# Kernel tuning notes

Hardware: AMD Instinct MI355X
Metric: run time of the kernel (lower is better)

Reference implementation:

```python
import jax, jax.numpy as jnp
import numpy as np

N_NODES = 2048
N_EDGES = 32768
D_IN = 128      # input_dimension
D_MEM_H = 128   # mem_hidden_dimension
D_MEM_A = 128   # mem_agg_hidden_dimension
D_AGG_H = 128   # agg_hidden_dimension
D_OUT = 128     # output_dimension
D_FEAT = 32     # feature_dimension


def setup_inputs() -> dict:
    key = jax.random.key(0)
    ks = jax.random.split(key, 10)
    state = jax.random.normal(ks[0], (N_EDGES, D_IN), dtype=jnp.float32)
    feature = jax.random.normal(ks[1], (N_EDGES, D_FEAT), dtype=jnp.float32)
    mask = (jax.random.uniform(ks[2], (N_NODES, N_EDGES)) < 0.005).astype(jnp.float32)
    mask_transpose = mask.T
    s = 0.05
    W1_m = jax.random.normal(ks[3], (D_MEM_H, D_IN), dtype=jnp.float32) * s
    b1_m = jax.random.normal(ks[4], (D_MEM_H,), dtype=jnp.float32) * s
    W2_m = jax.random.normal(ks[5], (D_MEM_A, D_MEM_H), dtype=jnp.float32) * s
    W1_a = jax.random.normal(ks[6], (D_AGG_H, D_MEM_A + D_FEAT), dtype=jnp.float32) * s
    b1_a = jax.random.normal(ks[7], (D_AGG_H,), dtype=jnp.float32) * s
    W2_a = jax.random.normal(ks[8], (D_OUT, D_AGG_H), dtype=jnp.float32) * s
    return {"state": state, "feature": feature, "mask": mask,
            "mask_transpose": mask_transpose,
            "W1_m": W1_m, "b1_m": b1_m, "W2_m": W2_m,
            "W1_a": W1_a, "b1_a": b1_a, "W2_a": W2_a}


def reference(state, feature, mask, mask_transpose, W1_m, b1_m, W2_m, W1_a, b1_a, W2_a):
    ls = jax.nn.log_sigmoid
    # memory MLP: [E, D_IN] -> [E, D_MEM_A]
    s = ls(ls(state @ W1_m.T + b1_m) @ W2_m.T)
    # bipartite aggregation: gather per-node sums, scatter back to edges
    agg = mask_transpose @ (mask @ s) - s  # include_self_message=False
    # concat features and aggregation MLP: [E, D_MEM_A + D_FEAT] -> [E, D_OUT]
    agg = jnp.concatenate((agg, feature), axis=1)
    out = ls(ls(agg @ W1_a.T + b1_a) @ W2_a.T)
    return out
```

## Files before the change

### kernel.cpp

```cpp
#include <hip/hip_runtime.h>
#include <cstdint>
#include <cstddef>

#define N_NODES 2048
#define N_EDGES 32768
#define ROW_CAP 384
#define COL_CAP 48

typedef unsigned short u16;
typedef __bf16 bf16x8 __attribute__((ext_vector_type(8)));
typedef float f32x4 __attribute__((ext_vector_type(4)));

union BF8 {
  bf16x8 v;
  u16 s[8];
  uint4 q;
};

__device__ __forceinline__ u16 f2bf(float f) {
  uint32_t u = __float_as_uint(f);
  uint32_t r = (u + 0x7fffu + ((u >> 16) & 1u)) >> 16;
  return (u16)r;
}
__device__ __forceinline__ float bf2f(u16 h) {
  return __uint_as_float(((uint32_t)h) << 16);
}
__device__ __forceinline__ float logsig(float x) {
  return fminf(x, 0.0f) - __logf(1.0f + __expf(-fabsf(x)));
}

__global__ __launch_bounds__(256) void conv_weights(
    const float* __restrict__ W1m, const float* __restrict__ W2m,
    const float* __restrict__ W1a, const float* __restrict__ W2a,
    u16* __restrict__ wb)
{
  const int i = blockIdx.x * 256 + threadIdx.x;
  if (i < 16384)      wb[i] = f2bf(W1m[i]);
  else if (i < 32768) wb[i] = f2bf(W2m[i - 16384]);
  else if (i < 53248) wb[i] = f2bf(W1a[i - 32768]);
  else if (i < 69632) wb[i] = f2bf(W2a[i - 53248]);
}

__global__ __launch_bounds__(256) void mlp_m_kernel(
    const float* __restrict__ state, const u16* __restrict__ W1b,
    const float* __restrict__ b1, const u16* __restrict__ W2b,
    u16* __restrict__ s_out)
{
  const int tid = threadIdx.x;
  const int wave = tid >> 6;
  const int lane = tid & 63;
  const int l16 = lane & 15;
  const int quad = lane >> 4;
  const int row0 = blockIdx.x * 128;

  __shared__ u16 h_lds[128][136];

  const f32x4 vzero = {0.f, 0.f, 0.f, 0.f};
  f32x4 acc[2][8];
  for (int rt = 0; rt < 2; ++rt)
    for (int ct = 0; ct < 8; ++ct) acc[rt][ct] = vzero;

  for (int kc = 0; kc < 4; ++kc) {
    const int k0 = kc * 32 + quad * 8;
    BF8 a[2];
    for (int rt = 0; rt < 2; ++rt) {
      const float* ap = state + (size_t)(row0 + wave * 32 + rt * 16 + l16) * 128 + k0;
      const float4 f0 = ((const float4*)ap)[0];
      const float4 f1 = ((const float4*)ap)[1];
      a[rt].s[0] = f2bf(f0.x); a[rt].s[1] = f2bf(f0.y);
      a[rt].s[2] = f2bf(f0.z); a[rt].s[3] = f2bf(f0.w);
      a[rt].s[4] = f2bf(f1.x); a[rt].s[5] = f2bf(f1.y);
      a[rt].s[6] = f2bf(f1.z); a[rt].s[7] = f2bf(f1.w);
    }
    for (int ct = 0; ct < 8; ++ct) {
      BF8 b;
      b.q = *(const uint4*)(W1b + (size_t)(ct * 16 + l16) * 128 + k0);
      for (int rt = 0; rt < 2; ++rt)
        acc[rt][ct] = __builtin_amdgcn_mfma_f32_16x16x32_bf16(a[rt].v, b.v, acc[rt][ct], 0, 0, 0);
    }
  }

  for (int ct = 0; ct < 8; ++ct) {
    const int col = ct * 16 + l16;
    const float bias = b1[col];
    for (int rt = 0; rt < 2; ++rt) {
      const int r = wave * 32 + rt * 16 + quad * 4;
      for (int i = 0; i < 4; ++i)
        h_lds[r + i][col] = f2bf(logsig(acc[rt][ct][i] + bias));
    }
  }
  __syncthreads();

  f32x4 acc2[2][8];
  for (int rt = 0; rt < 2; ++rt)
    for (int ct = 0; ct < 8; ++ct) acc2[rt][ct] = vzero;

  for (int kc = 0; kc < 4; ++kc) {
    const int k0 = kc * 32 + quad * 8;
    BF8 a[2];
    for (int rt = 0; rt < 2; ++rt)
      a[rt].q = *(const uint4*)&h_lds[wave * 32 + rt * 16 + l16][k0];
    for (int ct = 0; ct < 8; ++ct) {
      BF8 b;
      b.q = *(const uint4*)(W2b + (size_t)(ct * 16 + l16) * 128 + k0);
      for (int rt = 0; rt < 2; ++rt)
        acc2[rt][ct] = __builtin_amdgcn_mfma_f32_16x16x32_bf16(a[rt].v, b.v, acc2[rt][ct], 0, 0, 0);
    }
  }

  for (int ct = 0; ct < 8; ++ct) {
    const int col = ct * 16 + l16;
    for (int rt = 0; rt < 2; ++rt) {
      const int r = row0 + wave * 32 + rt * 16 + quad * 4;
      for (int i = 0; i < 4; ++i)
        s_out[(size_t)(r + i) * 128 + col] = f2bf(logsig(acc2[rt][ct][i]));
    }
  }
}

__global__ __launch_bounds__(256) void scan_mask(
    const float* __restrict__ mask, int* __restrict__ row_cnt,
    int* __restrict__ row_edges, int* __restrict__ col_cnt,
    int* __restrict__ col_nodes)
{
  const int n = blockIdx.x;
  __shared__ int cnt;
  __shared__ int list[ROW_CAP];
  if (threadIdx.x == 0) cnt = 0;
  __syncthreads();

  const uint4* row = (const uint4*)(mask + (size_t)n * N_EDGES);
  for (int i = threadIdx.x; i < N_EDGES / 4; i += 256) {
    const uint4 v = row[i];
    const int e = i * 4;
    if (v.x) { int p = atomicAdd(&cnt, 1); if (p < ROW_CAP) list[p] = e; }
    if (v.y) { int p = atomicAdd(&cnt, 1); if (p < ROW_CAP) list[p] = e + 1; }
    if (v.z) { int p = atomicAdd(&cnt, 1); if (p < ROW_CAP) list[p] = e + 2; }
    if (v.w) { int p = atomicAdd(&cnt, 1); if (p < ROW_CAP) list[p] = e + 3; }
  }
  __syncthreads();

  const int c = min(cnt, ROW_CAP);
  if (threadIdx.x == 0) row_cnt[n] = c;
  for (int i = threadIdx.x; i < c; i += 256) {
    const int e = list[i];
    row_edges[(size_t)n * ROW_CAP + i] = e;
    const int slot = atomicAdd(&col_cnt[e], 1);
    if (slot < COL_CAP) col_nodes[(size_t)e * COL_CAP + slot] = n;
  }
}

__global__ __launch_bounds__(128) void pass_a(
    const u16* __restrict__ s_bf, const int* __restrict__ row_cnt,
    const int* __restrict__ row_edges, float* __restrict__ y)
{
  const int n = blockIdx.x;
  const int d = threadIdx.x;
  __shared__ int elist[ROW_CAP];
  const int cnt = row_cnt[n];
  for (int i = threadIdx.x; i < cnt; i += 128)
    elist[i] = row_edges[(size_t)n * ROW_CAP + i];
  __syncthreads();
  float acc = 0.f;
#pragma unroll 4
  for (int i = 0; i < cnt; ++i)
    acc += bf2f(s_bf[(size_t)elist[i] * 128 + d]);
  y[n * 128 + d] = acc;
}

__global__ __launch_bounds__(256) void pass_b(
    const float* __restrict__ y, const u16* __restrict__ s_bf,
    const float* __restrict__ feature, const int* __restrict__ col_cnt,
    const int* __restrict__ col_nodes, u16* __restrict__ cat)
{
  const int e = blockIdx.x * 2 + (threadIdx.x >> 7);
  const int d = threadIdx.x & 127;
  const int cnt = min(col_cnt[e], COL_CAP);
  const int* cn = col_nodes + (size_t)e * COL_CAP;
  float acc = 0.f;
#pragma unroll 2
  for (int j = 0; j < cnt; ++j)
    acc += y[cn[j] * 128 + d];
  acc -= bf2f(s_bf[(size_t)e * 128 + d]);
  cat[(size_t)e * 160 + d] = f2bf(acc);
  if (d < 32)
    cat[(size_t)e * 160 + 128 + d] = f2bf(feature[e * 32 + d]);
}

__global__ __launch_bounds__(256) void mlp_a_kernel(
    const u16* __restrict__ cat, const u16* __restrict__ W1b,
    const float* __restrict__ b1, const u16* __restrict__ W2b,
    float* __restrict__ out)
{
  const int tid = threadIdx.x;
  const int wave = tid >> 6;
  const int lane = tid & 63;
  const int l16 = lane & 15;
  const int quad = lane >> 4;
  const int row0 = blockIdx.x * 128;

  __shared__ u16 h_lds[128][136];

  const f32x4 vzero = {0.f, 0.f, 0.f, 0.f};
  f32x4 acc[2][8];
  for (int rt = 0; rt < 2; ++rt)
    for (int ct = 0; ct < 8; ++ct) acc[rt][ct] = vzero;

  for (int kc = 0; kc < 5; ++kc) {
    const int k0 = kc * 32 + quad * 8;
    BF8 a[2];
    for (int rt = 0; rt < 2; ++rt)
      a[rt].q = *(const uint4*)(cat + (size_t)(row0 + wave * 32 + rt * 16 + l16) * 160 + k0);
    for (int ct = 0; ct < 8; ++ct) {
      BF8 b;
      b.q = *(const uint4*)(W1b + (size_t)(ct * 16 + l16) * 160 + k0);
      for (int rt = 0; rt < 2; ++rt)
        acc[rt][ct] = __builtin_amdgcn_mfma_f32_16x16x32_bf16(a[rt].v, b.v, acc[rt][ct], 0, 0, 0);
    }
  }

  for (int ct = 0; ct < 8; ++ct) {
    const int col = ct * 16 + l16;
    const float bias = b1[col];
    for (int rt = 0; rt < 2; ++rt) {
      const int r = wave * 32 + rt * 16 + quad * 4;
      for (int i = 0; i < 4; ++i)
        h_lds[r + i][col] = f2bf(logsig(acc[rt][ct][i] + bias));
    }
  }
  __syncthreads();

  f32x4 acc2[2][8];
  for (int rt = 0; rt < 2; ++rt)
    for (int ct = 0; ct < 8; ++ct) acc2[rt][ct] = vzero;

  for (int kc = 0; kc < 4; ++kc) {
    const int k0 = kc * 32 + quad * 8;
    BF8 a[2];
    for (int rt = 0; rt < 2; ++rt)
      a[rt].q = *(const uint4*)&h_lds[wave * 32 + rt * 16 + l16][k0];
    for (int ct = 0; ct < 8; ++ct) {
      BF8 b;
      b.q = *(const uint4*)(W2b + (size_t)(ct * 16 + l16) * 128 + k0);
      for (int rt = 0; rt < 2; ++rt)
        acc2[rt][ct] = __builtin_amdgcn_mfma_f32_16x16x32_bf16(a[rt].v, b.v, acc2[rt][ct], 0, 0, 0);
    }
  }

  for (int ct = 0; ct < 8; ++ct) {
    const int col = ct * 16 + l16;
    for (int rt = 0; rt < 2; ++rt) {
      const int r = row0 + wave * 32 + rt * 16 + quad * 4;
      for (int i = 0; i < 4; ++i)
        out[(size_t)(r + i) * 128 + col] = logsig(acc2[rt][ct][i]);
    }
  }
}

extern "C" void kernel_launch(void* const* d_in, const int* in_sizes, int n_in,
                              void* d_out, int out_size, void* d_ws, size_t ws_size,
                              hipStream_t stream)
{
  const float* state   = (const float*)d_in[0];
  const float* feature = (const float*)d_in[1];
  const float* mask    = (const float*)d_in[2];
  const float* W1m = (const float*)d_in[4];
  const float* b1m = (const float*)d_in[5];
  const float* W2m = (const float*)d_in[6];
  const float* W1a = (const float*)d_in[7];
  const float* b1a = (const float*)d_in[8];
  const float* W2a = (const float*)d_in[9];
  float* out = (float*)d_out;

  char* ws = (char*)d_ws;
  u16*  s_bf      = (u16*)(ws);
  u16*  cat       = (u16*)(ws + 8388608);
  float* y        = (float*)(ws + 18874368);
  int*  row_cnt   = (int*)(ws + 19922944);
  int*  row_edges = (int*)(ws + 19931136);
  int*  col_cnt   = (int*)(ws + 23076864);
  int*  col_nodes = (int*)(ws + 23207936);
  u16*  wb        = (u16*)(ws + 29499392);

  hipMemsetAsync(col_cnt, 0, N_EDGES * sizeof(int), stream);
  conv_weights<<<272, 256, 0, stream>>>(W1m, W2m, W1a, W2a, wb);
  mlp_m_kernel<<<N_EDGES / 128, 256, 0, stream>>>(state, wb, b1m, wb + 16384, s_bf);
  scan_mask<<<N_NODES, 256, 0, stream>>>(mask, row_cnt, row_edges, col_cnt, col_nodes);
  pass_a<<<N_NODES, 128, 0, stream>>>(s_bf, row_cnt, row_edges, y);
  pass_b<<<N_EDGES / 2, 256, 0, stream>>>(y, s_bf, feature, col_cnt, col_nodes, cat);
  mlp_a_kernel<<<N_EDGES / 128, 256, 0, stream>>>(cat, wb + 32768, b1a, wb + 53248, out);
}
```

Baseline: 623.4 us.

## Fuse mask scan with memory MLP and aggregation scatter with agg MLP

Merges the memory MLP and mask scanning into one heterogeneous launch so the two independent stages run concurrently. The per-edge gather of node sums is fused into the aggregation MLP and stays in LDS, so the concatenated tensor never goes to global memory. The memset is folded into the weight conversion kernel, the mask scan uses wave ballots with one atomic per wave and nontemporal loads, and pass_a splits each node's edge list across two thread halves. The cost is more LDS per block in agg_mlp, which may lower occupancy, and a less coalesced per-wave gather.

Measured after the change: 687.6 us. 10.3% more time.

```diff
diff --git a/kernel.cpp b/kernel.cpp
--- a/kernel.cpp
+++ b/kernel.cpp
@@ -10,6 +10,7 @@
 typedef unsigned short u16;
 typedef __bf16 bf16x8 __attribute__((ext_vector_type(8)));
 typedef float f32x4 __attribute__((ext_vector_type(4)));
+typedef uint32_t u32x4 __attribute__((ext_vector_type(4)));
 
 union BF8 {
   bf16x8 v;
@@ -32,49 +33,212 @@
 __global__ __launch_bounds__(256) void conv_weights(
     const float* __restrict__ W1m, const float* __restrict__ W2m,
     const float* __restrict__ W1a, const float* __restrict__ W2a,
-    u16* __restrict__ wb)
+    u16* __restrict__ wb, int* __restrict__ col_cnt)
 {
   const int i = blockIdx.x * 256 + threadIdx.x;
+  if (i < N_EDGES) col_cnt[i] = 0;
   if (i < 16384)      wb[i] = f2bf(W1m[i]);
   else if (i < 32768) wb[i] = f2bf(W2m[i - 16384]);
   else if (i < 53248) wb[i] = f2bf(W1a[i - 32768]);
   else if (i < 69632) wb[i] = f2bf(W2a[i - 53248]);
 }
 
-__global__ __launch_bounds__(256) void mlp_m_kernel(
+__global__ __launch_bounds__(256) void mlp_scan(
     const float* __restrict__ state, const u16* __restrict__ W1b,
     const float* __restrict__ b1, const u16* __restrict__ W2b,
-    u16* __restrict__ s_out)
+    u16* __restrict__ s_out,
+    const float* __restrict__ mask, int* __restrict__ row_cnt,
+    int* __restrict__ row_edges, int* __restrict__ col_cnt,
+    int* __restrict__ col_nodes)
+{
+  const int tid = threadIdx.x;
+
+  __shared__ u16 h_lds[128][136];
+  __shared__ int cnt;
+  __shared__ int list[ROW_CAP];
+
+  if (blockIdx.x < 256) {
+    const int wave = tid >> 6;
+    const int lane = tid & 63;
+    const int l16 = lane & 15;
+    const int quad = lane >> 4;
+    const int row0 = blockIdx.x * 128;
+
+    const f32x4 vzero = {0.f, 0.f, 0.f, 0.f};
+    f32x4 acc[2][8];
+    for (int rt = 0; rt < 2; ++rt)
+      for (int ct = 0; ct < 8; ++ct) acc[rt][ct] = vzero;
+
+    for (int kc = 0; kc < 4; ++kc) {
+      const int k0 = kc * 32 + quad * 8;
+      BF8 a[2];
+      for (int rt = 0; rt < 2; ++rt) {
+        const float* ap = state + (size_t)(row0 + wave * 32 + rt * 16 + l16) * 128 + k0;
+        const float4 f0 = ((const float4*)ap)[0];
+        const float4 f1 = ((const float4*)ap)[1];
+        a[rt].s[0] = f2bf(f0.x); a[rt].s[1] = f2bf(f0.y);
+        a[rt].s[2] = f2bf(f0.z); a[rt].s[3] = f2bf(f0.w);
+        a[rt].s[4] = f2bf(f1.x); a[rt].s[5] = f2bf(f1.y);
+        a[rt].s[6] = f2bf(f1.z); a[rt].s[7] = f2bf(f1.w);
+      }
+      for (int ct = 0; ct < 8; ++ct) {
+        BF8 b;
+        b.q = *(const uint4*)(W1b + (size_t)(ct * 16 + l16) * 128 + k0);
+        for (int rt = 0; rt < 2; ++rt)
+          acc[rt][ct] = __builtin_amdgcn_mfma_f32_16x16x32_bf16(a[rt].v, b.v, acc[rt][ct], 0, 0, 0);
+      }
+    }
+
+    for (int ct = 0; ct < 8; ++ct) {
+      const int col = ct * 16 + l16;
+      const float bias = b1[col];
+      for (int rt = 0; rt < 2; ++rt) {
+        const int r = wave * 32 + rt * 16 + quad * 4;
+        for (int i = 0; i < 4; ++i)
+          h_lds[r + i][col] = f2bf(logsig(acc[rt][ct][i] + bias));
+      }
+    }
+    __syncthreads();
+
+    f32x4 acc2[2][8];
+    for (int rt = 0; rt < 2; ++rt)
+      for (int ct = 0; ct < 8; ++ct) acc2[rt][ct] = vzero;
+
+    for (int kc = 0; kc < 4; ++kc) {
+      const int k0 = kc * 32 + quad * 8;
+      BF8 a[2];
+      for (int rt = 0; rt < 2; ++rt)
+        a[rt].q = *(const uint4*)&h_lds[wave * 32 + rt * 16 + l16][k0];
+      for (int ct = 0; ct < 8; ++ct) {
+        BF8 b;
+        b.q = *(const uint4*)(W2b + (size_t)(ct * 16 + l16) * 128 + k0);
+        for (int rt = 0; rt < 2; ++rt)
+          acc2[rt][ct] = __builtin_amdgcn_mfma_f32_16x16x32_bf16(a[rt].v, b.v, acc2[rt][ct], 0, 0, 0);
+      }
+    }
+
+    for (int ct = 0; ct < 8; ++ct) {
+      const int col = ct * 16 + l16;
+      for (int rt = 0; rt < 2; ++rt) {
+        const int r = row0 + wave * 32 + rt * 16 + quad * 4;
+        for (int i = 0; i < 4; ++i)
+          s_out[(size_t)(r + i) * 128 + col] = f2bf(logsig(acc2[rt][ct][i]));
+      }
+    }
+  } else {
+    const int n = blockIdx.x - 256;
+    const int lane = tid & 63;
+    if (tid == 0) cnt = 0;
+    __syncthreads();
+
+    const u32x4* row = (const u32x4*)(mask + (size_t)n * N_EDGES);
+    for (int i = tid; i < N_EDGES / 4; i += 256) {
+      const u32x4 v = __builtin_nontemporal_load(&row[i]);
+#pragma unroll
+      for (int k = 0; k < 4; ++k) {
+        const bool p = (v[k] != 0u);
+        const unsigned long long m = __ballot(p);
+        if (m) {
+          int base = 0;
+          if (lane == 0) base = atomicAdd(&cnt, __popcll(m));
+          base = __shfl(base, 0);
+          if (p) {
+            const int off = __popcll(m & ((1ull << lane) - 1ull));
+            if (base + off < ROW_CAP) list[base + off] = i * 4 + k;
+          }
+        }
+      }
+    }
+    __syncthreads();
+
+    const int c = min(cnt, ROW_CAP);
+    if (tid == 0) row_cnt[n] = c;
+    for (int i = tid; i < c; i += 256) {
+      const int e = list[i];
+      row_edges[(size_t)n * ROW_CAP + i] = e;
+      const int slot = atomicAdd(&col_cnt[e], 1);
+      if (slot < COL_CAP) col_nodes[(size_t)e * COL_CAP + slot] = n;
+    }
+  }
+}
+
+__global__ __launch_bounds__(256) void pass_a(
+    const u16* __restrict__ s_bf, const int* __restrict__ row_cnt,
+    const int* __restrict__ row_edges, float* __restrict__ y)
+{
+  const int n = blockIdx.x;
+  const int d = threadIdx.x & 127;
+  const int half = threadIdx.x >> 7;
+  __shared__ int elist[ROW_CAP];
+  __shared__ float part[128];
+  const int cnt = row_cnt[n];
+  for (int i = threadIdx.x; i < cnt; i += 256)
+    elist[i] = row_edges[(size_t)n * ROW_CAP + i];
+  __syncthreads();
+  float acc = 0.f;
+#pragma unroll 4
+  for (int i = half; i < cnt; i += 2)
+    acc += bf2f(s_bf[(size_t)elist[i] * 128 + d]);
+  if (half == 1) part[d] = acc;
+  __syncthreads();
+  if (half == 0) y[n * 128 + d] = acc + part[d];
+}
+
+__global__ __launch_bounds__(256) void agg_mlp(
+    const float* __restrict__ y, const u16* __restrict__ s_bf,
+    const float* __restrict__ feature, const int* __restrict__ col_cnt,
+    const int* __restrict__ col_nodes,
+    const u16* __restrict__ W1b, const float* __restrict__ b1,
+    const u16* __restrict__ W2b, float* __restrict__ out)
 {
   const int tid = threadIdx.x;
   const int wave = tid >> 6;
   const int lane = tid & 63;
+  const int row0 = blockIdx.x * 128;
+
+  __shared__ u16 cat[128][168];
+  __shared__ u16 h_lds[128][136];
+
+  const int d0 = lane * 2;
+  for (int it = 0; it < 32; ++it) {
+    const int le = it * 4 + wave;
+    const int e = row0 + le;
+    const int cnt = min(col_cnt[e], COL_CAP);
+    const int* cn = col_nodes + (size_t)e * COL_CAP;
+    float a0 = 0.f, a1 = 0.f;
+    for (int j = 0; j < cnt; ++j) {
+      const int nn = cn[j];
+      const float2 yv = *(const float2*)&y[nn * 128 + d0];
+      a0 += yv.x; a1 += yv.y;
+    }
+    const uint32_t sp = *(const uint32_t*)&s_bf[(size_t)e * 128 + d0];
+    a0 -= bf2f((u16)(sp & 0xffffu));
+    a1 -= bf2f((u16)(sp >> 16));
+    uint32_t packed = (uint32_t)f2bf(a0) | ((uint32_t)f2bf(a1) << 16);
+    *(uint32_t*)&cat[le][d0] = packed;
+    if (lane < 16) {
+      const float2 fv = *(const float2*)&feature[e * 32 + lane * 2];
+      uint32_t pf = (uint32_t)f2bf(fv.x) | ((uint32_t)f2bf(fv.y) << 16);
+      *(uint32_t*)&cat[le][128 + lane * 2] = pf;
+    }
+  }
+  __syncthreads();
+
   const int l16 = lane & 15;
   const int quad = lane >> 4;
-  const int row0 = blockIdx.x * 128;
-
-  __shared__ u16 h_lds[128][136];
-
   const f32x4 vzero = {0.f, 0.f, 0.f, 0.f};
   f32x4 acc[2][8];
   for (int rt = 0; rt < 2; ++rt)
     for (int ct = 0; ct < 8; ++ct) acc[rt][ct] = vzero;
 
-  for (int kc = 0; kc < 4; ++kc) {
+  for (int kc = 0; kc < 5; ++kc) {
     const int k0 = kc * 32 + quad * 8;
     BF8 a[2];
-    for (int rt = 0; rt < 2; ++rt) {
-      const float* ap = state + (size_t)(row0 + wave * 32 + rt * 16 + l16) * 128 + k0;
-      const float4 f0 = ((const float4*)ap)[0];
-      const float4 f1 = ((const float4*)ap)[1];
-      a[rt].s[0] = f2bf(f0.x); a[rt].s[1] = f2bf(f0.y);
-      a[rt].s[2] = f2bf(f0.z); a[rt].s[3] = f2bf(f0.w);
-      a[rt].s[4] = f2bf(f1.x); a[rt].s[5] = f2bf(f1.y);
-      a[rt].s[6] = f2bf(f1.z); a[rt].s[7] = f2bf(f1.w);
-    }
+    for (int rt = 0; rt < 2; ++rt)
+      a[rt].q = *(const uint4*)&cat[wave * 32 + rt * 16 + l16][k0];
     for (int ct = 0; ct < 8; ++ct) {
       BF8 b;
-      b.q = *(const uint4*)(W1b + (size_t)(ct * 16 + l16) * 128 + k0);
+      b.q = *(const uint4*)(W1b + (size_t)(ct * 16 + l16) * 160 + k0);
       for (int rt = 0; rt < 2; ++rt)
         acc[rt][ct] = __builtin_amdgcn_mfma_f32_16x16x32_bf16(a[rt].v, b.v, acc[rt][ct], 0, 0, 0);
     }
@@ -113,145 +277,6 @@
     for (int rt = 0; rt < 2; ++rt) {
       const int r = row0 + wave * 32 + rt * 16 + quad * 4;
       for (int i = 0; i < 4; ++i)
-        s_out[(size_t)(r + i) * 128 + col] = f2bf(logsig(acc2[rt][ct][i]));
-    }
-  }
-}
-
-__global__ __launch_bounds__(256) void scan_mask(
-    const float* __restrict__ mask, int* __restrict__ row_cnt,
-    int* __restrict__ row_edges, int* __restrict__ col_cnt,
-    int* __restrict__ col_nodes)
-{
-  const int n = blockIdx.x;
-  __shared__ int cnt;
-  __shared__ int list[ROW_CAP];
-  if (threadIdx.x == 0) cnt = 0;
-  __syncthreads();
-
-  const uint4* row = (const uint4*)(mask + (size_t)n * N_EDGES);
-  for (int i = threadIdx.x; i < N_EDGES / 4; i += 256) {
-    const uint4 v = row[i];
-    const int e = i * 4;
-    if (v.x) { int p = atomicAdd(&cnt, 1); if (p < ROW_CAP) list[p] = e; }
-    if (v.y) { int p = atomicAdd(&cnt, 1); if (p < ROW_CAP) list[p] = e + 1; }
-    if (v.z) { int p = atomicAdd(&cnt, 1); if (p < ROW_CAP) list[p] = e + 2; }
-    if (v.w) { int p = atomicAdd(&cnt, 1); if (p < ROW_CAP) list[p] = e + 3; }
-  }
-  __syncthreads();
-
-  const int c = min(cnt, ROW_CAP);
-  if (threadIdx.x == 0) row_cnt[n] = c;
-  for (int i = threadIdx.x; i < c; i += 256) {
-    const int e = list[i];
-    row_edges[(size_t)n * ROW_CAP + i] = e;
-    const int slot = atomicAdd(&col_cnt[e], 1);
-    if (slot < COL_CAP) col_nodes[(size_t)e * COL_CAP + slot] = n;
-  }
-}
-
-__global__ __launch_bounds__(128) void pass_a(
-    const u16* __restrict__ s_bf, const int* __restrict__ row_cnt,
-    const int* __restrict__ row_edges, float* __restrict__ y)
-{
-  const int n = blockIdx.x;
-  const int d = threadIdx.x;
-  __shared__ int elist[ROW_CAP];
-  const int cnt = row_cnt[n];
-  for (int i = threadIdx.x; i < cnt; i += 128)
-    elist[i] = row_edges[(size_t)n * ROW_CAP + i];
-  __syncthreads();
-  float acc = 0.f;
-#pragma unroll 4
-  for (int i = 0; i < cnt; ++i)
-    acc += bf2f(s_bf[(size_t)elist[i] * 128 + d]);
-  y[n * 128 + d] = acc;
-}
-
-__global__ __launch_bounds__(256) void pass_b(
-    const float* __restrict__ y, const u16* __restrict__ s_bf,
-    const float* __restrict__ feature, const int* __restrict__ col_cnt,
-    const int* __restrict__ col_nodes, u16* __restrict__ cat)
-{
-  const int e = blockIdx.x * 2 + (threadIdx.x >> 7);
-  const int d = threadIdx.x & 127;
-  const int cnt = min(col_cnt[e], COL_CAP);
-  const int* cn = col_nodes + (size_t)e * COL_CAP;
-  float acc = 0.f;
-#pragma unroll 2
-  for (int j = 0; j < cnt; ++j)
-    acc += y[cn[j] * 128 + d];
-  acc -= bf2f(s_bf[(size_t)e * 128 + d]);
-  cat[(size_t)e * 160 + d] = f2bf(acc);
-  if (d < 32)
-    cat[(size_t)e * 160 + 128 + d] = f2bf(feature[e * 32 + d]);
-}
-
-__global__ __launch_bounds__(256) void mlp_a_kernel(
-    const u16* __restrict__ cat, const u16* __restrict__ W1b,
-    const float* __restrict__ b1, const u16* __restrict__ W2b,
-    float* __restrict__ out)
-{
-  const int tid = threadIdx.x;
-  const int wave = tid >> 6;
-  const int lane = tid & 63;
-  const int l16 = lane & 15;
-  const int quad = lane >> 4;
-  const int row0 = blockIdx.x * 128;
-
-  __shared__ u16 h_lds[128][136];
-
-  const f32x4 vzero = {0.f, 0.f, 0.f, 0.f};
-  f32x4 acc[2][8];
-  for (int rt = 0; rt < 2; ++rt)
-    for (int ct = 0; ct < 8; ++ct) acc[rt][ct] = vzero;
-
-  for (int kc = 0; kc < 5; ++kc) {
-    const int k0 = kc * 32 + quad * 8;
-    BF8 a[2];
-    for (int rt = 0; rt < 2; ++rt)
-      a[rt].q = *(const uint4*)(cat + (size_t)(row0 + wave * 32 + rt * 16 + l16) * 160 + k0);
-    for (int ct = 0; ct < 8; ++ct) {
-      BF8 b;
-      b.q = *(const uint4*)(W1b + (size_t)(ct * 16 + l16) * 160 + k0);
-      for (int rt = 0; rt < 2; ++rt)
-        acc[rt][ct] = __builtin_amdgcn_mfma_f32_16x16x32_bf16(a[rt].v, b.v, acc[rt][ct], 0, 0, 0);
-    }
-  }
-
-  for (int ct = 0; ct < 8; ++ct) {
-    const int col = ct * 16 + l16;
-    const float bias = b1[col];
-    for (int rt = 0; rt < 2; ++rt) {
-      const int r = wave * 32 + rt * 16 + quad * 4;
-      for (int i = 0; i < 4; ++i)
-        h_lds[r + i][col] = f2bf(logsig(acc[rt][ct][i] + bias));
-    }
-  }
-  __syncthreads();
-
-  f32x4 acc2[2][8];
-  for (int rt = 0; rt < 2; ++rt)
-    for (int ct = 0; ct < 8; ++ct) acc2[rt][ct] = vzero;
-
-  for (int kc = 0; kc < 4; ++kc) {
-    const int k0 = kc * 32 + quad * 8;
-    BF8 a[2];
-    for (int rt = 0; rt < 2; ++rt)
-      a[rt].q = *(const uint4*)&h_lds[wave * 32 + rt * 16 + l16][k0];
-    for (int ct = 0; ct < 8; ++ct) {
-      BF8 b;
-      b.q = *(const uint4*)(W2b + (size_t)(ct * 16 + l16) * 128 + k0);
-      for (int rt = 0; rt < 2; ++rt)
-        acc2[rt][ct] = __builtin_amdgcn_mfma_f32_16x16x32_bf16(a[rt].v, b.v, acc2[rt][ct], 0, 0, 0);
-    }
-  }
-
-  for (int ct = 0; ct < 8; ++ct) {
-    const int col = ct * 16 + l16;
-    for (int rt = 0; rt < 2; ++rt) {
-      const int r = row0 + wave * 32 + rt * 16 + quad * 4;
-      for (int i = 0; i < 4; ++i)
         out[(size_t)(r + i) * 128 + col] = logsig(acc2[rt][ct][i]);
     }
   }
@@ -274,19 +299,17 @@
 
   char* ws = (char*)d_ws;
   u16*  s_bf      = (u16*)(ws);
-  u16*  cat       = (u16*)(ws + 8388608);
-  float* y        = (float*)(ws + 18874368);
-  int*  row_cnt   = (int*)(ws + 19922944);
-  int*  row_edges = (int*)(ws + 19931136);
-  int*  col_cnt   = (int*)(ws + 23076864);
-  int*  col_nodes = (int*)(ws + 23207936);
-  u16*  wb        = (u16*)(ws + 29499392);
-
-  hipMemsetAsync(col_cnt, 0, N_EDGES * sizeof(int), stream);
-  conv_weights<<<272, 256, 0, stream>>>(W1m, W2m, W1a, W2a, wb);
-  mlp_m_kernel<<<N_EDGES / 128, 256, 0, stream>>>(state, wb, b1m, wb + 16384, s_bf);
-  scan_mask<<<N_NODES, 256, 0, stream>>>(mask, row_cnt, row_edges, col_cnt, col_nodes);
-  pass_a<<<N_NODES, 128, 0, stream>>>(s_bf, row_cnt, row_edges, y);
-  pass_b<<<N_EDGES / 2, 256, 0, stream>>>(y, s_bf, feature, col_cnt, col_nodes, cat);
-  mlp_a_kernel<<<N_EDGES / 128, 256, 0, stream>>>(cat, wb + 32768, b1a, wb + 53248, out);
-}
+  float* y        = (float*)(ws + 8388608);
+  int*  row_cnt   = (int*)(ws + 9437184);
+  int*  row_edges = (int*)(ws + 9445376);
+  int*  col_cnt   = (int*)(ws + 12591104);
+  int*  col_nodes = (int*)(ws + 12722176);
+  u16*  wb        = (u16*)(ws + 19013632);
+
+  conv_weights<<<272, 256, 0, stream>>>(W1m, W2m, W1a, W2a, wb, col_cnt);
+  mlp_scan<<<256 + N_NODES, 256, 0, stream>>>(state, wb, b1m, wb + 16384, s_bf,
+                                              mask, row_cnt, row_edges, col_cnt, col_nodes);
+  pass_a<<<N_NODES, 256, 0, stream>>>(s_bf, row_cnt, row_edges, y);
+  agg_mlp<<<N_EDGES / 128, 256, 0, stream>>>(y, s_bf, feature, col_cnt, col_nodes,
+                                             wb + 32768, b1a, wb + 53248, out);
+}
```
